# Kernel tuning notes

Hardware: AMD Instinct MI355X
Metric: run time of the kernel (lower is better)

Reference implementation:

```python
import math
import jax, jax.numpy as jnp
import numpy as np

NUM_HEAD = 16

def get_slopes(n):
    def pow2(n):
        start = 2 ** (-(2 ** (-(math.log2(n) - 3))))
        return [start * start ** i for i in range(n)]
    if math.log2(n).is_integer():
        return pow2(n)
    c = 2 ** math.floor(math.log2(n))
    return pow2(c) + get_slopes(2 * c)[0::2][: n - c]

def setup_inputs() -> dict:
    key = jax.random.key(0)
    ks = jax.random.split(key, 5)
    B, T, D = 2, 2048, 1024
    x = jax.random.normal(ks[0], (B, T, D), dtype=jnp.float32)
    Wq = jax.random.normal(ks[1], (D, D), dtype=jnp.float32) * 0.02
    Wk = jax.random.normal(ks[2], (D, D), dtype=jnp.float32) * 0.02
    Wv = jax.random.normal(ks[3], (D, D), dtype=jnp.float32) * 0.02
    Wo = jax.random.normal(ks[4], (D, D), dtype=jnp.float32) * (0.02 / math.sqrt(2 * 24))
    return {"x": x, "Wq": Wq, "Wk": Wk, "Wv": Wv, "Wo": Wo}

def reference(x, Wq, Wk, Wv, Wo):
    B, T, D = x.shape
    H = NUM_HEAD
    hd = D // H
    # projections (no bias)
    q = (x @ Wq).reshape(B, T, H, hd).transpose(0, 2, 1, 3)  # b h t d
    k = (x @ Wk).reshape(B, T, H, hd).transpose(0, 2, 1, 3)
    v = (x @ Wv).reshape(B, T, H, hd).transpose(0, 2, 1, 3)
    scores = jnp.einsum("bhqd,bhkd->bhqk", q, k) / jnp.sqrt(jnp.asarray(hd, dtype=q.dtype))
    # ALiBi bias: slopes[h] * (j - (T-1)), broadcast over query positions
    slopes = jnp.asarray(np.array(get_slopes(H), dtype=np.float32))
    alibi = slopes[:, None, None] * (jnp.arange(T, dtype=jnp.float32) - (T - 1))[None, None, :]  # h 1 k
    scores = scores + alibi[None]  # b h q k
    causal = jnp.tril(jnp.ones((T, T), dtype=bool))
    masked = jnp.where(causal[None, None], scores.astype(jnp.float32), jnp.finfo(jnp.float32).min)
    p = jax.nn.softmax(masked, axis=-1)
    attn_out = jnp.einsum("bhqk,bhkd->bhqd", p, v)
    attn_out = attn_out.transpose(0, 2, 1, 3).reshape(B, T, D)
    return attn_out @ Wo
```

## Files before the change

### kernel.cpp

```cpp
#include <hip/hip_runtime.h>
#include <hip/hip_bf16.h>
#include <math.h>

#define B_ 2
#define T_ 2048
#define D_ 1024
#define H_ 16
#define HD 64

typedef __bf16 bf16;
typedef bf16 bf16x8 __attribute__((ext_vector_type(8)));
typedef bf16 bf16x4 __attribute__((ext_vector_type(4)));
typedef short short4v __attribute__((ext_vector_type(4)));
typedef float f32x4 __attribute__((ext_vector_type(4)));

#define GL2LDS16(g, l) __builtin_amdgcn_global_load_lds(                      \
    (const __attribute__((address_space(1))) void*)(g),                       \
    (__attribute__((address_space(3))) void*)(l), 16, 0, 0)

static __device__ __forceinline__ f32x4 mfma16x16x16(bf16x4 a, bf16x4 b, f32x4 c) {
#if defined(__HIP_DEVICE_COMPILE__)
# if __has_builtin(__builtin_amdgcn_mfma_f32_16x16x16bf16_1k)
    return __builtin_amdgcn_mfma_f32_16x16x16bf16_1k(
        __builtin_bit_cast(short4v, a), __builtin_bit_cast(short4v, b), c, 0, 0, 0);
# else
    asm("v_mfma_f32_16x16x16_bf16 %0, %1, %2, %0" : "+v"(c) : "v"(a), "v"(b));
    return c;
# endif
#else
    (void)a; (void)b;
    return c;
#endif
}

static __device__ __forceinline__ bf16x4 lo4(bf16x8 v) {
    return __builtin_shufflevector(v, v, 0, 1, 2, 3);
}
static __device__ __forceinline__ bf16x4 hi4(bf16x8 v) {
    return __builtin_shufflevector(v, v, 4, 5, 6, 7);
}

__global__ __launch_bounds__(256) void prep_inputs(const float* __restrict__ x,
                                                   const float* __restrict__ W0,
                                                   const float* __restrict__ W1,
                                                   const float* __restrict__ W2,
                                                   const float* __restrict__ W3,
                                                   bf16* __restrict__ xb,
                                                   bf16* __restrict__ Wt) {
    const int z = blockIdx.z;
    const int tid = threadIdx.x;
    if (z >= 4) {
        size_t i = ((((size_t)(z - 4) * 256 + blockIdx.y * 16 + blockIdx.x) * 256) + tid) * 4;
        float4 v = *(const float4*)(x + i);
        bf16 tmp[4] = {(bf16)v.x, (bf16)v.y, (bf16)v.z, (bf16)v.w};
        *(uint2*)(xb + i) = *(const uint2*)tmp;
        return;
    }
    __shared__ bf16 tile[64 * 72];
    const float* W = (z == 0) ? W0 : (z == 1) ? W1 : (z == 2) ? W2 : W3;
    bf16* out = Wt + (size_t)z * D_ * D_;
    const int k0 = blockIdx.y * 64, n0 = blockIdx.x * 64;
    for (int it = 0; it < 4; ++it) {
        int idx = it * 256 + tid;
        int r = idx >> 4;
        int c4 = (idx & 15) << 2;
        float4 v = *(const float4*)(W + (size_t)(k0 + r) * D_ + n0 + c4);
        tile[(c4 + 0) * 72 + r] = (bf16)v.x;
        tile[(c4 + 1) * 72 + r] = (bf16)v.y;
        tile[(c4 + 2) * 72 + r] = (bf16)v.z;
        tile[(c4 + 3) * 72 + r] = (bf16)v.w;
    }
    __syncthreads();
    for (int it = 0; it < 2; ++it) {
        int idx = it * 256 + tid;
        int r = idx >> 3;
        int c8 = (idx & 7) << 3;
        bf16x8 v = *(const bf16x8*)&tile[r * 72 + c8];
        *(bf16x8*)(out + (size_t)(n0 + r) * D_ + k0 + c8) = v;
    }
}

__global__ __launch_bounds__(256) void gemm_qkv(const bf16* __restrict__ A,
                                                const bf16* __restrict__ Bt,
                                                bf16* __restrict__ Cout) {
    __shared__ bf16 As[2][128 * 32];
    __shared__ bf16 Bs[3][2][64 * 32];
    const int bid = blockIdx.x;
    const int xcd = bid & 7, rr = bid >> 3;
    const int y   = (xcd << 2) + (rr & 3);
    const int xx  = rr >> 2;
    const int m0 = y * 128, n0 = xx * 64;

    const int tid = threadIdx.x;
    const int wave = tid >> 6, lane = tid & 63;
    const int quad = lane >> 4, l16 = lane & 15;
    const int wr = wave >> 1, wc = wave & 1;

    const int lrow = lane >> 2, lcol = (lane & 3) << 3;
    const bf16* ag = A + (size_t)(m0 + wave * 32 + lrow) * D_ + lcol;
    const size_t brow = (size_t)(n0 + wave * 16 + lrow) * D_ + lcol;
    const int a_off = (wave * 32 + lrow) * 32 + lcol;
    const int b_off = (wave * 16 + lrow) * 32 + lcol;

    f32x4 acc[3][4][2];
#pragma unroll
    for (int z = 0; z < 3; ++z)
#pragma unroll
        for (int mi = 0; mi < 4; ++mi)
#pragma unroll
            for (int ni = 0; ni < 2; ++ni) acc[z][mi][ni] = (f32x4){0.f, 0.f, 0.f, 0.f};

    for (int kb = 0; kb < D_; kb += 64) {
        GL2LDS16(ag + kb,                        &As[0][a_off]);
        GL2LDS16(ag + (size_t)16 * D_ + kb,      &As[0][a_off + 16 * 32]);
        GL2LDS16(ag + kb + 32,                   &As[1][a_off]);
        GL2LDS16(ag + (size_t)16 * D_ + kb + 32, &As[1][a_off + 16 * 32]);
#pragma unroll
        for (int z = 0; z < 3; ++z) {
            const bf16* bg = Bt + (size_t)z * D_ * D_ + brow;
            GL2LDS16(bg + kb,      &Bs[z][0][b_off]);
            GL2LDS16(bg + kb + 32, &Bs[z][1][b_off]);
        }
        __syncthreads();

#pragma unroll
        for (int half = 0; half < 2; ++half) {
            bf16x8 af[4];
#pragma unroll
            for (int mi = 0; mi < 4; ++mi)
                af[mi] = *(const bf16x8*)&As[half][(wr * 64 + mi * 16 + l16) * 32 + quad * 8];
#pragma unroll
            for (int z = 0; z < 3; ++z) {
                bf16x8 bfr[2];
#pragma unroll
                for (int ni = 0; ni < 2; ++ni)
                    bfr[ni] = *(const bf16x8*)&Bs[z][half][(wc * 32 + ni * 16 + l16) * 32 + quad * 8];
                if (z < 2) {
#pragma unroll
                    for (int mi = 0; mi < 4; ++mi)
#pragma unroll
                        for (int ni = 0; ni < 2; ++ni)
                            acc[z][mi][ni] = __builtin_amdgcn_mfma_f32_16x16x32_bf16(
                                bfr[ni], af[mi], acc[z][mi][ni], 0, 0, 0);
                } else {
#pragma unroll
                    for (int mi = 0; mi < 4; ++mi)
#pragma unroll
                        for (int ni = 0; ni < 2; ++ni)
                            acc[z][mi][ni] = __builtin_amdgcn_mfma_f32_16x16x32_bf16(
                                af[mi], bfr[ni], acc[z][mi][ni], 0, 0, 0);
                }
            }
        }
        __syncthreads();
    }

#pragma unroll
    for (int z = 0; z < 3; ++z) {
        bf16* Cb = Cout + (size_t)z * (B_ * T_) * D_;
        const float qscale = (z == 0) ? 0.180336887f : 1.0f;
        if (z < 2) {
#pragma unroll
            for (int mi = 0; mi < 4; ++mi)
#pragma unroll
                for (int ni = 0; ni < 2; ++ni) {
                    int m = m0 + wr * 64 + mi * 16 + l16;
                    int n = n0 + wc * 32 + ni * 16 + quad * 4;
                    int b = m >> 11, t = m & (T_ - 1);
                    int h = n >> 6, d = n & (HD - 1);
                    bf16 o4[4];
                    for (int r = 0; r < 4; ++r) o4[r] = (bf16)(acc[z][mi][ni][r] * qscale);
                    *(uint2*)&Cb[(((((size_t)b * H_ + h) * T_ + t) << 6) + d)] =
                        *(const uint2*)o4;
                }
        } else {
#pragma unroll
            for (int mi = 0; mi < 4; ++mi)
#pragma unroll
                for (int ni = 0; ni < 2; ++ni) {
                    int m = m0 + wr * 64 + mi * 16 + quad * 4;
                    int n = n0 + wc * 32 + ni * 16 + l16;
                    int b = m >> 11, t = m & (T_ - 1);
                    int h = n >> 6, d = n & (HD - 1);
                    bf16 o4[4];
                    for (int r = 0; r < 4; ++r) o4[r] = (bf16)acc[z][mi][ni][r];
                    *(uint2*)&Cb[((((size_t)b * H_ + h) * HD + d) * T_ + t)] =
                        *(const uint2*)o4;
                }
        }
    }
}

__global__ __launch_bounds__(256) void gemm_out(const bf16* __restrict__ A,
                                                const bf16* __restrict__ Bt,
                                                float* __restrict__ Cout) {
    __shared__ bf16 As[2][128 * 32];
    __shared__ bf16 Bs[2][64 * 32];
    const int bid = blockIdx.x;
    const int xcd = bid & 7, rr = bid >> 3;
    const int y   = (xcd << 2) + (rr & 3);
    const int xx  = rr >> 2;
    const int m0 = y * 128, n0 = xx * 64;

    const int tid = threadIdx.x;
    const int wave = tid >> 6, lane = tid & 63;
    const int quad = lane >> 4, l16 = lane & 15;
    const int wr = wave >> 1, wc = wave & 1;

    const int lrow = lane >> 2, lcol = (lane & 3) << 3;
    const bf16* ag = A  + (size_t)(m0 + wave * 32 + lrow) * D_ + lcol;
    const bf16* bg = Bt + (size_t)(n0 + wave * 16 + lrow) * D_ + lcol;
    const int a_off = (wave * 32 + lrow) * 32 + lcol;
    const int b_off = (wave * 16 + lrow) * 32 + lcol;

    f32x4 acc[4][2];
    for (int mi = 0; mi < 4; ++mi)
        for (int ni = 0; ni < 2; ++ni) acc[mi][ni] = (f32x4){0.f, 0.f, 0.f, 0.f};

    for (int kb = 0; kb < D_; kb += 64) {
        GL2LDS16(ag + kb,                        &As[0][a_off]);
        GL2LDS16(ag + (size_t)16 * D_ + kb,      &As[0][a_off + 16 * 32]);
        GL2LDS16(ag + kb + 32,                   &As[1][a_off]);
        GL2LDS16(ag + (size_t)16 * D_ + kb + 32, &As[1][a_off + 16 * 32]);
        GL2LDS16(bg + kb,                        &Bs[0][b_off]);
        GL2LDS16(bg + kb + 32,                   &Bs[1][b_off]);
        __syncthreads();

        for (int half = 0; half < 2; ++half) {
            bf16x8 af[4], bfr[2];
            for (int mi = 0; mi < 4; ++mi)
                af[mi] = *(const bf16x8*)&As[half][(wr * 64 + mi * 16 + l16) * 32 + quad * 8];
            for (int ni = 0; ni < 2; ++ni)
                bfr[ni] = *(const bf16x8*)&Bs[half][(wc * 32 + ni * 16 + l16) * 32 + quad * 8];
            for (int mi = 0; mi < 4; ++mi)
                for (int ni = 0; ni < 2; ++ni)
                    acc[mi][ni] = __builtin_amdgcn_mfma_f32_16x16x32_bf16(
                        bfr[ni], af[mi], acc[mi][ni], 0, 0, 0);
        }
        __syncthreads();
    }

    for (int mi = 0; mi < 4; ++mi)
        for (int ni = 0; ni < 2; ++ni) {
            int m = m0 + wr * 64 + mi * 16 + l16;
            int n = n0 + wc * 32 + ni * 16 + quad * 4;
            *(f32x4*)&Cout[(size_t)m * D_ + n] = acc[mi][ni];
        }
}

__device__ __constant__ unsigned char ITEM_QT[24] = {
    8,9,10,11,12,13,14,15, 7,15, 6,14, 5,13, 4,12, 3,11, 2,10, 1,9, 0,8};
__device__ __constant__ unsigned char ITEM_KIND[24] = {
    1,1,1,1,1,1,1,1, 0,2, 0,2, 0,2, 0,2, 0,2, 0,2, 0,2, 0,2};

#define LDK 72
#define LDP 136

struct KVStage { bf16x8 k0, k1, v0, v1; };

__global__ __launch_bounds__(512, 4) void attn_kernel(const bf16* __restrict__ Q,
                                                      const bf16* __restrict__ K,
                                                      const bf16* __restrict__ Vt,
                                                      bf16* __restrict__ O,
                                                      float* __restrict__ Opart,
                                                      float2* __restrict__ ML) {
    __shared__ bf16 Ks[128 * LDK];
    __shared__ bf16 Vs[64 * LDP];

    const int bh = blockIdx.x;
    const int item = blockIdx.y;
    const int qt = ITEM_QT[item];
    const int kind = ITEM_KIND[item];
    const int h = bh & (H_ - 1), b = bh >> 4;
    const int tid = threadIdx.x;
    const int wave = tid >> 6, lane = tid & 63;
    const int quad = lane >> 4, l16 = lane & 15;

    const bf16* Qb = Q + (size_t)bh * T_ * HD;
    const bf16* Kb = K + (size_t)bh * T_ * HD;
    const bf16* Vb = Vt + (size_t)bh * HD * T_;

    const float slope2 = exp2f(-0.5f * (float)(h + 1)) * 1.44269504f;

    bf16x8 qf[2];
    {
        const bf16* qrow = Qb + (size_t)(qt * 128 + wave * 16 + l16) * HD + quad * 8;
        qf[0] = *(const bf16x8*)(qrow);
        qf[1] = *(const bf16x8*)(qrow + 32);
    }

    const int slot0 = tid, slot1 = 512 + tid;
    const int rk0 = slot0 >> 3, ck0 = (slot0 & 7) << 3;
    const int rk1 = slot1 >> 3, ck1 = (slot1 & 7) << 3;
    const int rv0 = slot0 >> 4, c0 = slot0 & 15;
    const int rv1 = slot1 >> 4, c1 = slot1 & 15;
    const int vs0 = rv0 * LDP + (c0 & 1) * 64 + (c0 >> 1) * 4;
    const int vs1 = rv1 * LDP + (c1 & 1) * 64 + (c1 >> 1) * 4;

    auto loadKV = [&](int t, KVStage& st) {
        const bf16* kb = Kb + (size_t)t * 128 * HD;
        st.k0 = *(const bf16x8*)(kb + rk0 * HD + ck0);
        st.k1 = *(const bf16x8*)(kb + rk1 * HD + ck1);
        const bf16* vb = Vb + t * 128;
        st.v0 = *(const bf16x8*)(vb + (size_t)rv0 * T_ + c0 * 8);
        st.v1 = *(const bf16x8*)(vb + (size_t)rv1 * T_ + c1 * 8);
    };
    auto storeKV = [&](const KVStage& st) {
        *(bf16x8*)&Ks[rk0 * LDK + ck0] = st.k0;
        *(bf16x8*)&Ks[rk1 * LDK + ck1] = st.k1;
        *(bf16x4*)&Vs[vs0]      = lo4(st.v0);
        *(bf16x4*)&Vs[vs0 + 32] = hi4(st.v0);
        *(bf16x4*)&Vs[vs1]      = lo4(st.v1);
        *(bf16x4*)&Vs[vs1 + 32] = hi4(st.v1);
    };

    f32x4 acc[4];
    for (int df = 0; df < 4; ++df) acc[df] = (f32x4){0.f, 0.f, 0.f, 0.f};
    float m_run = -INFINITY, l_lane = 0.f;

    const int qglob = qt * 128 + wave * 16 + l16;
    const int nkt = qt + 1;
    const int kt0 = (kind == 2) ? 8 : 0;
    const int kt1 = (kind == 1) ? 8 : nkt;

    auto compute = [&](int kt, bool last) {
        f32x4 s[8];
#pragma unroll
        for (int nf = 0; nf < 8; ++nf) {
            bf16x8 kf0 = *(const bf16x8*)&Ks[(nf * 16 + l16) * LDK + quad * 8];
            bf16x8 kf1 = *(const bf16x8*)&Ks[(nf * 16 + l16) * LDK + 32 + quad * 8];
            f32x4 zz = (f32x4){0.f, 0.f, 0.f, 0.f};
            __builtin_amdgcn_s_setprio(1);
            zz = __builtin_amdgcn_mfma_f32_16x16x32_bf16(kf0, qf[0], zz, 0, 0, 0);
            zz = __builtin_amdgcn_mfma_f32_16x16x32_bf16(kf1, qf[1], zz, 0, 0, 0);
            __builtin_amdgcn_s_setprio(0);
            s[nf] = zz;
        }

        const float j0f = (float)(kt * 128 + quad * 4 - (T_ - 1));
#pragma unroll
        for (int nf = 0; nf < 8; ++nf)
#pragma unroll
            for (int r = 0; r < 4; ++r)
                s[nf][r] += slope2 * (j0f + (float)(nf * 16 + r));
        if (last) {
            const int jb = kt * 128 + quad * 4;
#pragma unroll
            for (int nf = 0; nf < 8; ++nf)
#pragma unroll
                for (int r = 0; r < 4; ++r)
                    if (jb + nf * 16 + r > qglob) s[nf][r] = -INFINITY;
        }

        float a[8];
#pragma unroll
        for (int nf = 0; nf < 8; ++nf)
            a[nf] = fmaxf(fmaxf(s[nf][0], s[nf][1]), fmaxf(s[nf][2], s[nf][3]));
        float t0 = fmaxf(a[0], a[1]), t1 = fmaxf(a[2], a[3]);
        float t2 = fmaxf(a[4], a[5]), t3 = fmaxf(a[6], a[7]);
        float mx = fmaxf(fmaxf(t0, t1), fmaxf(t2, t3));
        mx = fmaxf(mx, __shfl_xor(mx, 16, 64));
        mx = fmaxf(mx, __shfl_xor(mx, 32, 64));

        if (!__all(mx - m_run <= 8.f)) {
            const float mnew = fmaxf(m_run, mx);
            const float alpha = exp2f(m_run - mnew);
            l_lane *= alpha;
#pragma unroll
            for (int df = 0; df < 4; ++df) acc[df] *= alpha;
            m_run = mnew;
        }

        float rs0 = 0.f, rs1 = 0.f;
        bf16x4 pf[8];
#pragma unroll
        for (int nf = 0; nf < 8; ++nf) {
            float p0 = exp2f(s[nf][0] - m_run);
            float p1 = exp2f(s[nf][1] - m_run);
            float p2 = exp2f(s[nf][2] - m_run);
            float p3 = exp2f(s[nf][3] - m_run);
            if (nf & 1) rs1 += (p0 + p1) + (p2 + p3);
            else        rs0 += (p0 + p1) + (p2 + p3);
            pf[nf] = (bf16x4){(bf16)p0, (bf16)p1, (bf16)p2, (bf16)p3};
        }
        l_lane += rs0 + rs1;

#pragma unroll
        for (int j = 0; j < 4; ++j) {
            bf16x8 w[4];
#pragma unroll
            for (int df = 0; df < 4; ++df)
                w[df] = *(const bf16x8*)&Vs[(df * 16 + l16) * LDP + quad * 32 + j * 8];
            __builtin_amdgcn_s_setprio(1);
#pragma unroll
            for (int df = 0; df < 4; ++df) {
                acc[df] = mfma16x16x16(lo4(w[df]), pf[2 * j],     acc[df]);
                acc[df] = mfma16x16x16(hi4(w[df]), pf[2 * j + 1], acc[df]);
            }
            __builtin_amdgcn_s_setprio(0);
        }
    };

    KVStage sA, sB;
    loadKV(kt0, sA);
    int kt = kt0;
    for (;;) {
        __syncthreads();
        storeKV(sA);
        if (kt + 1 < kt1) loadKV(kt + 1, sB);
        __syncthreads();
        compute(kt, kt == nkt - 1);
        if (++kt >= kt1) break;
        __syncthreads();
        storeKV(sB);
        if (kt + 1 < kt1) loadKV(kt + 1, sA);
        __syncthreads();
        compute(kt, kt == nkt - 1);
        if (++kt >= kt1) break;
    }

    float l_run = l_lane;
    l_run += __shfl_xor(l_run, 16, 64);
    l_run += __shfl_xor(l_run, 32, 64);

    if (kind == 0) {
        const float inv = 1.0f / l_run;
        for (int df = 0; df < 4; ++df) {
            bf16 o4[4];
            for (int r = 0; r < 4; ++r) o4[r] = (bf16)(acc[df][r] * inv);
            *(uint2*)&O[(((size_t)b * T_ + qglob) * H_ + h) * HD + df * 16 + quad * 4] =
                *(const uint2*)o4;
        }
    } else {
        const int pidx = (bh * 8 + (qt - 8)) * 2 + (kind == 2 ? 1 : 0);
        const int ql = wave * 16 + l16;
        float* dst = Opart + (size_t)pidx * 8192 + ql * 64;
        for (int df = 0; df < 4; ++df)
            *(f32x4*)&dst[df * 16 + quad * 4] = acc[df];
        if (quad == 0) ML[pidx * 128 + ql] = make_float2(m_run, l_run);
    }
}

__global__ __launch_bounds__(512) void attn_merge(const float* __restrict__ Opart,
                                                  const float2* __restrict__ ML,
                                                  bf16* __restrict__ O) {
    const int qt = 8 + blockIdx.x, bh = blockIdx.y;
    const int h = bh & (H_ - 1), b = bh >> 4;
    const int tid = threadIdx.x;
    const int q = tid >> 2, dc = (tid & 3) << 4;
    const int p0 = (bh * 8 + blockIdx.x) * 2, p1 = p0 + 1;

    const float2 ml0 = ML[p0 * 128 + q], ml1 = ML[p1 * 128 + q];
    const float M = fmaxf(ml0.x, ml1.x);
    const float e0 = exp2f(ml0.x - M), e1 = exp2f(ml1.x - M);
    const float inv = 1.0f / (e0 * ml0.y + e1 * ml1.y);

    const float* a = Opart + (size_t)p0 * 8192 + q * 64 + dc;
    const float* c = Opart + (size_t)p1 * 8192 + q * 64 + dc;
    bf16 o16[16];
    for (int j = 0; j < 4; ++j) {
        f32x4 va = *(const f32x4*)(a + j * 4);
        f32x4 vc = *(const f32x4*)(c + j * 4);
        for (int r = 0; r < 4; ++r)
            o16[j * 4 + r] = (bf16)((va[r] * e0 + vc[r] * e1) * inv);
    }
    const int t = qt * 128 + q;
    bf16* dst = O + (((size_t)b * T_ + t) * H_ + h) * HD + dc;
    *(bf16x8*)dst = *(const bf16x8*)o16;
    *(bf16x8*)(dst + 8) = *(const bf16x8*)(o16 + 8);
}

extern "C" void kernel_launch(void* const* d_in, const int* in_sizes, int n_in,
                              void* d_out, int out_size, void* d_ws, size_t ws_size,
                              hipStream_t stream) {
    const float* x  = (const float*)d_in[0];
    const float* Wq = (const float*)d_in[1];
    const float* Wk = (const float*)d_in[2];
    const float* Wv = (const float*)d_in[3];
    const float* Wo = (const float*)d_in[4];
    float* out = (float*)d_out;

    const size_t M = (size_t)B_ * T_;
    const size_t XE = M * D_;
    const size_t WE = (size_t)D_ * D_;

    char* ws = (char*)d_ws;
    size_t off = 0;
    auto carve = [&](size_t bytes) {
        void* p = ws + off;
        off += (bytes + 255) & ~(size_t)255;
        return p;
    };
    bf16* xb  = (bf16*)carve(XE * 2);
    bf16* Wt  = (bf16*)carve(4 * WE * 2);
    bf16* QKV = (bf16*)carve(3 * XE * 2);
    float*  Opart = (float*)carve(32 * 8 * 2 * 8192 * sizeof(float));
    float2* MLbuf = (float2*)carve(32 * 8 * 2 * 128 * sizeof(float2));
    bf16* attn = xb;

    prep_inputs<<<dim3(16, 16, 20), 256, 0, stream>>>(x, Wq, Wk, Wv, Wo, xb, Wt);

    gemm_qkv<<<512, 256, 0, stream>>>(xb, Wt, QKV);
    attn_kernel<<<dim3(32, 24), 512, 0, stream>>>(QKV, QKV + XE, QKV + 2 * XE,
                                                  attn, Opart, MLbuf);
    attn_merge<<<dim3(8, 32), 512, 0, stream>>>(Opart, MLbuf, attn);
    gemm_out<<<512, 256, 0, stream>>>(attn, Wt + 3 * WE, out);
}
```

Measured before the change: 189.4 us.

## Double-buffer LDS tiles in QKV and output GEMMs to overlap loads with MFMA

Both projection GEMMs now keep two LDS buffers. The next K-tile is issued with global_load_lds before the MFMA work on the current buffer runs, so each iteration needs one barrier instead of a load-then-sync-then-compute sequence. This aims to hide global memory latency behind matrix compute. The cost is double the LDS footprint (about 80KB per block for the QKV kernel), which can lower occupancy. The output GEMM's inner loops also get explicit unroll pragmas.

```diff
diff --git a/kernel.cpp b/kernel.cpp
--- a/kernel.cpp
+++ b/kernel.cpp
@@ -83,8 +83,8 @@
 __global__ __launch_bounds__(256) void gemm_qkv(const bf16* __restrict__ A,
                                                 const bf16* __restrict__ Bt,
                                                 bf16* __restrict__ Cout) {
-    __shared__ bf16 As[2][128 * 32];
-    __shared__ bf16 Bs[3][2][64 * 32];
+    __shared__ bf16 As[2][2][128 * 32];
+    __shared__ bf16 Bs[2][3][2][64 * 32];
     const int bid = blockIdx.x;
     const int xcd = bid & 7, rr = bid >> 3;
     const int y   = (xcd << 2) + (rr & 3);
@@ -110,31 +110,36 @@
 #pragma unroll
             for (int ni = 0; ni < 2; ++ni) acc[z][mi][ni] = (f32x4){0.f, 0.f, 0.f, 0.f};
 
-    for (int kb = 0; kb < D_; kb += 64) {
-        GL2LDS16(ag + kb,                        &As[0][a_off]);
-        GL2LDS16(ag + (size_t)16 * D_ + kb,      &As[0][a_off + 16 * 32]);
-        GL2LDS16(ag + kb + 32,                   &As[1][a_off]);
-        GL2LDS16(ag + (size_t)16 * D_ + kb + 32, &As[1][a_off + 16 * 32]);
+    auto stage = [&](int buf, int kb) {
+        GL2LDS16(ag + kb,                        &As[buf][0][a_off]);
+        GL2LDS16(ag + (size_t)16 * D_ + kb,      &As[buf][0][a_off + 16 * 32]);
+        GL2LDS16(ag + kb + 32,                   &As[buf][1][a_off]);
+        GL2LDS16(ag + (size_t)16 * D_ + kb + 32, &As[buf][1][a_off + 16 * 32]);
 #pragma unroll
         for (int z = 0; z < 3; ++z) {
             const bf16* bg = Bt + (size_t)z * D_ * D_ + brow;
-            GL2LDS16(bg + kb,      &Bs[z][0][b_off]);
-            GL2LDS16(bg + kb + 32, &Bs[z][1][b_off]);
-        }
-        __syncthreads();
-
+            GL2LDS16(bg + kb,      &Bs[buf][z][0][b_off]);
+            GL2LDS16(bg + kb + 32, &Bs[buf][z][1][b_off]);
+        }
+    };
+
+    stage(0, 0);
+    __syncthreads();
+    int cur = 0;
+    for (int kb = 0; kb < D_; kb += 64) {
+        if (kb + 64 < D_) stage(cur ^ 1, kb + 64);
 #pragma unroll
         for (int half = 0; half < 2; ++half) {
             bf16x8 af[4];
 #pragma unroll
             for (int mi = 0; mi < 4; ++mi)
-                af[mi] = *(const bf16x8*)&As[half][(wr * 64 + mi * 16 + l16) * 32 + quad * 8];
+                af[mi] = *(const bf16x8*)&As[cur][half][(wr * 64 + mi * 16 + l16) * 32 + quad * 8];
 #pragma unroll
             for (int z = 0; z < 3; ++z) {
                 bf16x8 bfr[2];
 #pragma unroll
                 for (int ni = 0; ni < 2; ++ni)
-                    bfr[ni] = *(const bf16x8*)&Bs[z][half][(wc * 32 + ni * 16 + l16) * 32 + quad * 8];
+                    bfr[ni] = *(const bf16x8*)&Bs[cur][z][half][(wc * 32 + ni * 16 + l16) * 32 + quad * 8];
                 if (z < 2) {
 #pragma unroll
                     for (int mi = 0; mi < 4; ++mi)
@@ -153,6 +158,7 @@
             }
         }
         __syncthreads();
+        cur ^= 1;
     }
 
 #pragma unroll
@@ -194,8 +200,8 @@
 __global__ __launch_bounds__(256) void gemm_out(const bf16* __restrict__ A,
                                                 const bf16* __restrict__ Bt,
                                                 float* __restrict__ Cout) {
-    __shared__ bf16 As[2][128 * 32];
-    __shared__ bf16 Bs[2][64 * 32];
+    __shared__ bf16 As[2][2][128 * 32];
+    __shared__ bf16 Bs[2][2][64 * 32];
     const int bid = blockIdx.x;
     const int xcd = bid & 7, rr = bid >> 3;
     const int y   = (xcd << 2) + (rr & 3);
@@ -217,27 +223,38 @@
     for (int mi = 0; mi < 4; ++mi)
         for (int ni = 0; ni < 2; ++ni) acc[mi][ni] = (f32x4){0.f, 0.f, 0.f, 0.f};
 
+    auto stage = [&](int buf, int kb) {
+        GL2LDS16(ag + kb,                        &As[buf][0][a_off]);
+        GL2LDS16(ag + (size_t)16 * D_ + kb,      &As[buf][0][a_off + 16 * 32]);
+        GL2LDS16(ag + kb + 32,                   &As[buf][1][a_off]);
+        GL2LDS16(ag + (size_t)16 * D_ + kb + 32, &As[buf][1][a_off + 16 * 32]);
+        GL2LDS16(bg + kb,                        &Bs[buf][0][b_off]);
+        GL2LDS16(bg + kb + 32,                   &Bs[buf][1][b_off]);
+    };
+
+    stage(0, 0);
+    __syncthreads();
+    int cur = 0;
     for (int kb = 0; kb < D_; kb += 64) {
-        GL2LDS16(ag + kb,                        &As[0][a_off]);
-        GL2LDS16(ag + (size_t)16 * D_ + kb,      &As[0][a_off + 16 * 32]);
-        GL2LDS16(ag + kb + 32,                   &As[1][a_off]);
-        GL2LDS16(ag + (size_t)16 * D_ + kb + 32, &As[1][a_off + 16 * 32]);
-        GL2LDS16(bg + kb,                        &Bs[0][b_off]);
-        GL2LDS16(bg + kb + 32,                   &Bs[1][b_off]);
-        __syncthreads();
-
+        if (kb + 64 < D_) stage(cur ^ 1, kb + 64);
+#pragma unroll
         for (int half = 0; half < 2; ++half) {
             bf16x8 af[4], bfr[2];
+#pragma unroll
             for (int mi = 0; mi < 4; ++mi)
-                af[mi] = *(const bf16x8*)&As[half][(wr * 64 + mi * 16 + l16) * 32 + quad * 8];
+                af[mi] = *(const bf16x8*)&As[cur][half][(wr * 64 + mi * 16 + l16) * 32 + quad * 8];
+#pragma unroll
             for (int ni = 0; ni < 2; ++ni)
-                bfr[ni] = *(const bf16x8*)&Bs[half][(wc * 32 + ni * 16 + l16) * 32 + quad * 8];
+                bfr[ni] = *(const bf16x8*)&Bs[cur][half][(wc * 32 + ni * 16 + l16) * 32 + quad * 8];
+#pragma unroll
             for (int mi = 0; mi < 4; ++mi)
+#pragma unroll
                 for (int ni = 0; ni < 2; ++ni)
                     acc[mi][ni] = __builtin_amdgcn_mfma_f32_16x16x32_bf16(
                         bfr[ni], af[mi], acc[mi][ni], 0, 0, 0);
         }
         __syncthreads();
+        cur ^= 1;
     }
 
     for (int mi = 0; mi < 4; ++mi)
```

After: 189.5 us. About the same (+0.0%).
